# Optimization experiments

Hardware: AMD Instinct MI355X
Metric: run time of the kernel (lower is better)

The kernel has to match this reference:

```python
import jax, jax.numpy as jnp
import numpy as np

N = 100000   # total nodes in batched graph
E = 400000   # directed edges
F0 = 64      # Drug_Features
B = 512      # number of graphs
FINAL = 128  # Final_dim


def setup_inputs() -> dict:
    key = jax.random.key(0)
    ks = jax.random.split(key, 24)
    def w(k, shape, fan_in):
        return jax.random.normal(k, shape, dtype=jnp.float32) / np.sqrt(fan_in)
    inp = {
        "x": jax.random.normal(ks[0], (N, F0), dtype=jnp.float32),
        "edge_index": jax.random.randint(ks[1], (2, E), 0, N, dtype=jnp.int32),
        "batch": jnp.sort(jax.random.randint(ks[2], (N,), 0, B, dtype=jnp.int32)),
        "eps": jax.random.normal(ks[3], (N, 4 * F0), dtype=jnp.float32),
        # GCNConv weights: lin (in,out) no bias, separate bias added post-aggregation
        "W1": w(ks[4], (F0, 2 * F0), F0), "b1": jnp.zeros((2 * F0,), jnp.float32),
        "W2": w(ks[5], (2 * F0, 3 * F0), 2 * F0), "b2": jnp.zeros((3 * F0,), jnp.float32),
        "W3": w(ks[6], (3 * F0, 4 * F0), 3 * F0), "b3": jnp.zeros((4 * F0,), jnp.float32),
        "Wmu": w(ks[7], (4 * F0, 4 * F0), 4 * F0), "bmu": jnp.zeros((4 * F0,), jnp.float32),
        "Wlv": w(ks[8], (4 * F0, 4 * F0), 4 * F0), "blv": jnp.zeros((4 * F0,), jnp.float32),
        "fc1_w": w(ks[9], (4 * F0, 1024), 4 * F0), "fc1_b": jnp.zeros((1024,), jnp.float32),
        "fc2_w": w(ks[10], (1024, FINAL), 1024), "fc2_b": jnp.zeros((FINAL,), jnp.float32),
    }
    return inp


def reference(x, edge_index, batch, eps, W1, b1, W2, b2, W3, b3, Wmu, bmu, Wlv, blv,
              fc1_w, fc1_b, fc2_w, fc2_b):
    n = x.shape[0]
    row, col = edge_index[0], edge_index[1]
    loop = jnp.arange(n, dtype=row.dtype)
    row_f = jnp.concatenate([row, loop])  # with self-loops (PyG GCNConv default)
    col_f = jnp.concatenate([col, loop])
    deg = jax.ops.segment_sum(jnp.ones_like(col_f, dtype=x.dtype), col_f, num_segments=n)
    dinv = jnp.where(deg > 0, deg ** -0.5, 0.0)
    norm = (dinv[row_f] * dinv[col_f])[:, None]  # [E+N, 1]

    def gcn(h, W, b):
        m = h @ W                                   # transform first (out <= in here ok)
        agg = jax.ops.segment_sum(norm * m[row_f], col_f, num_segments=n)
        return agg + b

    h = jax.nn.relu(gcn(x, W1, b1))
    h = jax.nn.relu(gcn(h, W2, b2))
    h = jax.nn.relu(gcn(h, W3, b3))   # PMVO pre-pool features [N, 4F]
    mu = gcn(h, Wmu, bmu)
    logvar = gcn(h, Wlv, blv)
    std = jnp.exp(0.5 * logvar)
    amvo = mu + eps * std             # reparameterize
    x2 = jax.ops.segment_max(h, batch, num_segments=B)   # global max pool per graph
    pmvo = jax.nn.relu(x2 @ fc1_w + fc1_b) @ fc2_w + fc2_b  # dropout is identity (eval)
    return (amvo, mu, logvar, pmvo)
```

## Files before the change

kernel.cpp:

```cpp
#include <hip/hip_runtime.h>
#include <hip/hip_bf16.h>
#include <math.h>


#define THREADS 256

typedef short s8v __attribute__((ext_vector_type(8)));
typedef float f4v __attribute__((ext_vector_type(4)));

__device__ inline float bf_lo(unsigned int u) {
    union { unsigned int i; float f; } c; c.i = u << 16; return c.f;
}
__device__ inline float bf_hi(unsigned int u) {
    union { unsigned int i; float f; } c; c.i = u & 0xffff0000u; return c.f;
}
__device__ inline unsigned short f2bf(float f) {
    __hip_bfloat16 h = __float2bfloat16(f);
    return *reinterpret_cast<unsigned short*>(&h);
}
__device__ inline float bf2f(unsigned short u) {
    union { unsigned int i; float f; } c; c.i = ((unsigned int)u) << 16; return c.f;
}


__global__ void k_count(const int* __restrict__ col, int* __restrict__ counts, int E) {
    int e = blockIdx.x * blockDim.x + threadIdx.x;
    if (e < E) atomicAdd(&counts[col[e]], 1);
}

__global__ void k_dinv(const int* __restrict__ counts, float* __restrict__ dinv, int N) {
    int i = blockIdx.x * blockDim.x + threadIdx.x;
    if (i < N) dinv[i] = rsqrtf((float)(counts[i] + 1));
}

__global__ __launch_bounds__(1024) void k_scan(const int* __restrict__ counts,
                                               int* __restrict__ offsets, int N) {
    __shared__ int ssum[1024];
    int tid = threadIdx.x;
    int chunk = (N + 1023) / 1024;
    int begin = tid * chunk;
    int end = begin + chunk; if (end > N) end = N;
    int s = 0;
    for (int i = begin; i < end; ++i) s += counts[i] + 1;
    ssum[tid] = s;
    __syncthreads();
    for (int off = 1; off < 1024; off <<= 1) {
        int v = 0;
        if (tid >= off) v = ssum[tid - off];
        __syncthreads();
        if (tid >= off) ssum[tid] += v;
        __syncthreads();
    }
    int prefix = (tid == 0) ? 0 : ssum[tid - 1];
    for (int i = begin; i < end; ++i) {
        offsets[i] = prefix;
        prefix += counts[i] + 1;
    }
    if (end == N && begin < N) offsets[N] = prefix;
}

__global__ void k_init_cursor(const int* __restrict__ offsets, int* __restrict__ cursor, int N) {
    int i = blockIdx.x * blockDim.x + threadIdx.x;
    if (i < N) cursor[i] = offsets[i];
}

__global__ void k_scatter(const int* __restrict__ row, const int* __restrict__ col,
                          const float* __restrict__ dinv, int* __restrict__ cursor,
                          int* __restrict__ csr_row, float* __restrict__ csr_norm,
                          int E, int N) {
    int e = blockIdx.x * blockDim.x + threadIdx.x;
    if (e < E) {
        int r = row[e], c = col[e];
        int slot = atomicAdd(&cursor[c], 1);
        csr_row[slot] = r;
        csr_norm[slot] = dinv[r] * dinv[c];
    } else if (e < E + N) {
        int i = e - E;
        int slot = atomicAdd(&cursor[i], 1);
        csr_row[slot] = i;
        float d = dinv[i];
        csr_norm[slot] = d * d;
    }
}


__global__ void k_cast_bf16(const float* __restrict__ src, unsigned short* __restrict__ dst, int n) {
    int i = blockIdx.x * blockDim.x + threadIdx.x;
    if (i < n) dst[i] = f2bf(src[i]);
}

__global__ void k_prep_w(const float* __restrict__ W, unsigned short* __restrict__ WT,
                         int K, int Nc) {
    int id = blockIdx.x * blockDim.x + threadIdx.x;
    if (id < K * Nc) {
        int k = id / Nc, n = id % Nc;
        WT[(size_t)n * K + k] = f2bf(W[id]);
    }
}

__global__ void k_agg(const unsigned short* __restrict__ h,
                      const int* __restrict__ offsets,
                      const int* __restrict__ csr_row,
                      const float* __restrict__ csr_nrm,
                      unsigned short* __restrict__ g, int N, int F) {
    int node = blockIdx.x * blockDim.y + threadIdx.y;
    if (node >= N) return;
    int c8 = threadIdx.x * 8;
    int off0 = offsets[node], off1 = offsets[node + 1];
    float a0=0.f,a1=0.f,a2=0.f,a3=0.f,a4=0.f,a5=0.f,a6=0.f,a7=0.f;
    for (int sl = off0; sl < off1; ++sl) {
        int r = csr_row[sl];
        float w = csr_nrm[sl];
        uint4 v = *(const uint4*)(h + (size_t)r * F + c8);
        a0 += w * bf_lo(v.x); a1 += w * bf_hi(v.x);
        a2 += w * bf_lo(v.y); a3 += w * bf_hi(v.y);
        a4 += w * bf_lo(v.z); a5 += w * bf_hi(v.z);
        a6 += w * bf_lo(v.w); a7 += w * bf_hi(v.w);
    }
    uint4 o;
    o.x = (unsigned)f2bf(a0) | ((unsigned)f2bf(a1) << 16);
    o.y = (unsigned)f2bf(a2) | ((unsigned)f2bf(a3) << 16);
    o.z = (unsigned)f2bf(a4) | ((unsigned)f2bf(a5) << 16);
    o.w = (unsigned)f2bf(a6) | ((unsigned)f2bf(a7) << 16);
    *(uint4*)(g + (size_t)node * F + c8) = o;
}

#define GBM 128
#define GBN 64
#define GBK 64
#define LDP 72

__global__ __launch_bounds__(256) void k_gemm_mfma(
    const unsigned short* __restrict__ A,
    const unsigned short* __restrict__ WT,
    const float* __restrict__ bias,
    void* __restrict__ Cout, int M, int K, int Nc,
    int dorelu, int out_bf16) {
    __shared__ unsigned short sA[GBM * LDP];
    __shared__ unsigned short sB[GBN * LDP];
    const int tid = threadIdx.x;
    const int wave = tid >> 6;
    const int lane = tid & 63;
    const int bm = blockIdx.x * GBM;
    const int bn = blockIdx.y * GBN;

    f4v acc[2][4];
    #pragma unroll
    for (int i = 0; i < 2; ++i)
        #pragma unroll
        for (int j = 0; j < 4; ++j) acc[i][j] = (f4v){0.f, 0.f, 0.f, 0.f};

    const int lrow = tid >> 3;
    const int lk = (tid & 7) * 8;
    const int fr = lane & 15;
    const int fk = (lane >> 4) * 8;

    for (int k0 = 0; k0 < K; k0 += GBK) {
        #pragma unroll
        for (int p = 0; p < 4; ++p) {
            int r = lrow + p * 32;
            int gm = bm + r;
            uint4 v = make_uint4(0u, 0u, 0u, 0u);
            if (gm < M) v = *(const uint4*)(A + (size_t)gm * K + k0 + lk);
            *(uint4*)(&sA[r * LDP + lk]) = v;
        }
        #pragma unroll
        for (int p = 0; p < 2; ++p) {
            int n = lrow + p * 32;
            uint4 v = *(const uint4*)(WT + (size_t)(bn + n) * K + k0 + lk);
            *(uint4*)(&sB[n * LDP + lk]) = v;
        }
        __syncthreads();
        #pragma unroll
        for (int ks = 0; ks < 2; ++ks) {
            s8v a0 = *(const s8v*)(&sA[(wave * 32 + fr) * LDP + ks * 32 + fk]);
            s8v a1 = *(const s8v*)(&sA[(wave * 32 + 16 + fr) * LDP + ks * 32 + fk]);
            #pragma unroll
            for (int nt = 0; nt < 4; ++nt) {
                s8v b = *(const s8v*)(&sB[(nt * 16 + fr) * LDP + ks * 32 + fk]);
                acc[0][nt] = __builtin_amdgcn_mfma_f32_16x16x32_bf16(a0, b, acc[0][nt], 0, 0, 0);
                acc[1][nt] = __builtin_amdgcn_mfma_f32_16x16x32_bf16(a1, b, acc[1][nt], 0, 0, 0);
            }
        }
        __syncthreads();
    }

    const int col_l = lane & 15;
    const int row_q = (lane >> 4) * 4;
    #pragma unroll
    for (int mt = 0; mt < 2; ++mt) {
        #pragma unroll
        for (int nt = 0; nt < 4; ++nt) {
            #pragma unroll
            for (int i = 0; i < 4; ++i) {
                int row = bm + wave * 32 + mt * 16 + row_q + i;
                int col = bn + nt * 16 + col_l;
                if (row < M) {
                    float v = acc[mt][nt][i] + bias[col];
                    if (dorelu) v = fmaxf(v, 0.f);
                    if (out_bf16)
                        ((unsigned short*)Cout)[(size_t)row * Nc + col] = f2bf(v);
                    else
                        ((float*)Cout)[(size_t)row * Nc + col] = v;
                }
            }
        }
    }
}

__global__ __launch_bounds__(256) void k_fc1(const float* __restrict__ x2,
                                             const float* __restrict__ W,
                                             const float* __restrict__ bias,
                                             float* __restrict__ hid,
                                             int K, int Nc) {
    const int m = blockIdx.x;
    const int t = threadIdx.x;
    __shared__ float sx[256];
    for (int k = t; k < K; k += 256) sx[k] = x2[(size_t)m * K + k];
    __syncthreads();
    const int nc4 = Nc >> 2;
    const float4* Wv = (const float4*)W;
    float4 acc = make_float4(0.f, 0.f, 0.f, 0.f);
    #pragma unroll 4
    for (int k = 0; k < K; ++k) {
        float a = sx[k];
        float4 w = Wv[(size_t)k * nc4 + t];
        acc.x += a * w.x; acc.y += a * w.y;
        acc.z += a * w.z; acc.w += a * w.w;
    }
    float4 b = ((const float4*)bias)[t];
    float4 r;
    r.x = fmaxf(acc.x + b.x, 0.f);
    r.y = fmaxf(acc.y + b.y, 0.f);
    r.z = fmaxf(acc.z + b.z, 0.f);
    r.w = fmaxf(acc.w + b.w, 0.f);
    ((float4*)hid)[(size_t)m * nc4 + t] = r;
}

__global__ __launch_bounds__(128) void k_fc2(const float* __restrict__ hid,
                                             const float* __restrict__ W,
                                             const float* __restrict__ bias,
                                             float* __restrict__ out,
                                             int K, int Nc) {
    const int m = blockIdx.x;
    const int c = threadIdx.x;
    __shared__ float sh[1024];
    for (int k = c; k < K; k += 128) sh[k] = hid[(size_t)m * K + k];
    __syncthreads();
    float a0 = 0.f, a1 = 0.f, a2 = 0.f, a3 = 0.f;
    for (int k = 0; k < K; k += 4) {
        a0 += sh[k    ] * W[(size_t)(k    ) * Nc + c];
        a1 += sh[k + 1] * W[(size_t)(k + 1) * Nc + c];
        a2 += sh[k + 2] * W[(size_t)(k + 2) * Nc + c];
        a3 += sh[k + 3] * W[(size_t)(k + 3) * Nc + c];
    }
    out[(size_t)m * Nc + c] = (a0 + a1) + (a2 + a3) + bias[c];
}


__global__ void k_amvo(const float* __restrict__ mu, const float* __restrict__ lv,
                       const float* __restrict__ eps, float* __restrict__ out, size_t n) {
    size_t i = (size_t)blockIdx.x * blockDim.x + threadIdx.x;
    if (i < n) out[i] = mu[i] + eps[i] * expf(0.5f * lv[i]);
}

__global__ void k_gstart(const int* __restrict__ batch, int* __restrict__ gstart, int Nn, int B) {
    int b = blockIdx.x * blockDim.x + threadIdx.x;
    if (b > B) return;
    int lo = 0, hi = Nn;
    while (lo < hi) {
        int mid = (lo + hi) >> 1;
        if (batch[mid] < b) lo = mid + 1; else hi = mid;
    }
    gstart[b] = lo;
}

__global__ void k_pool_max(const unsigned short* __restrict__ h, const int* __restrict__ gstart,
                           float* __restrict__ x2, int F) {
    int b = blockIdx.x;
    int s = gstart[b], e = gstart[b + 1];
    for (int c = threadIdx.x; c < F; c += blockDim.x) {
        float mv = -INFINITY;
        for (int i = s; i < e; ++i) mv = fmaxf(mv, bf2f(h[(size_t)i * F + c]));
        x2[(size_t)b * F + c] = mv;
    }
}

static inline int ceil_div(int a, int b) { return (a + b - 1) / b; }

extern "C" void kernel_launch(void* const* d_in, const int* in_sizes, int n_in,
                              void* d_out, int out_size, void* d_ws, size_t ws_size,
                              hipStream_t stream) {
    const int F0 = 64;
    const int N = in_sizes[0] / F0;
    const int E = in_sizes[1] / 2;
    const int F4 = 4 * F0;
    const int B = (out_size - 3 * N * F4) / 128;
    const int M = E + N;

    const float* x     = (const float*)d_in[0];
    const int*   ei    = (const int*)d_in[1];
    const int*   batch = (const int*)d_in[2];
    const float* eps   = (const float*)d_in[3];
    const float* W1  = (const float*)d_in[4];  const float* b1  = (const float*)d_in[5];
    const float* W2  = (const float*)d_in[6];  const float* b2  = (const float*)d_in[7];
    const float* W3  = (const float*)d_in[8];  const float* b3  = (const float*)d_in[9];
    const float* Wmu = (const float*)d_in[10]; const float* bmu = (const float*)d_in[11];
    const float* Wlv = (const float*)d_in[12]; const float* blv = (const float*)d_in[13];
    const float* fc1w = (const float*)d_in[14]; const float* fc1b = (const float*)d_in[15];
    const float* fc2w = (const float*)d_in[16]; const float* fc2b = (const float*)d_in[17];

    const int* e_row = ei;
    const int* e_col = ei + E;

    float* out  = (float*)d_out;
    float* amvo = out;
    float* mu   = out + (size_t)N * F4;
    float* lv   = out + 2 * (size_t)N * F4;
    float* pmvo = out + 3 * (size_t)N * F4;

    char* w = (char*)d_ws;
    auto alloc = [&](size_t bytes) -> void* {
        void* p = (void*)w;
        w += (bytes + 255) & ~(size_t)255;
        return p;
    };
    float* dinv    = (float*)alloc((size_t)N * 4);
    int*   counts  = (int*)alloc((size_t)N * 4);
    int*   offsets = (int*)alloc((size_t)(N + 1) * 4);
    int*   csr_row = (int*)alloc((size_t)M * 4);
    float* csr_nrm = (float*)alloc((size_t)M * 4);
    int*   gstart  = (int*)alloc((size_t)(B + 1) * 4);
    unsigned short* xb  = (unsigned short*)alloc((size_t)N * F0 * 2);
    unsigned short* h1  = (unsigned short*)alloc((size_t)N * 128 * 2);
    unsigned short* h2  = (unsigned short*)alloc((size_t)N * 192 * 2);
    unsigned short* h3  = (unsigned short*)alloc((size_t)N * 256 * 2);
    unsigned short* g   = (unsigned short*)alloc((size_t)N * 256 * 2);
    unsigned short* wt1 = (unsigned short*)alloc((size_t)64 * 128 * 2);
    unsigned short* wt2 = (unsigned short*)alloc((size_t)128 * 192 * 2);
    unsigned short* wt3 = (unsigned short*)alloc((size_t)192 * 256 * 2);
    unsigned short* wtm = (unsigned short*)alloc((size_t)256 * 256 * 2);
    unsigned short* wtl = (unsigned short*)alloc((size_t)256 * 256 * 2);
    float* x2  = (float*)alloc((size_t)B * F4 * 4);
    float* hid = (float*)alloc((size_t)B * 1024 * 4);
    (void)ws_size; (void)n_in;

    hipMemsetAsync(counts, 0, (size_t)N * 4, stream);
    k_count<<<ceil_div(E, THREADS), THREADS, 0, stream>>>(e_col, counts, E);
    k_dinv<<<ceil_div(N, THREADS), THREADS, 0, stream>>>(counts, dinv, N);
    k_scan<<<1, 1024, 0, stream>>>(counts, offsets, N);
    k_init_cursor<<<ceil_div(N, THREADS), THREADS, 0, stream>>>(offsets, counts, N);
    k_scatter<<<ceil_div(E + N, THREADS), THREADS, 0, stream>>>(
        e_row, e_col, dinv, counts, csr_row, csr_nrm, E, N);

    k_cast_bf16<<<ceil_div(N * F0, THREADS), THREADS, 0, stream>>>(x, xb, N * F0);
    k_prep_w<<<ceil_div(64 * 128, THREADS), THREADS, 0, stream>>>(W1, wt1, 64, 128);
    k_prep_w<<<ceil_div(128 * 192, THREADS), THREADS, 0, stream>>>(W2, wt2, 128, 192);
    k_prep_w<<<ceil_div(192 * 256, THREADS), THREADS, 0, stream>>>(W3, wt3, 192, 256);
    k_prep_w<<<ceil_div(256 * 256, THREADS), THREADS, 0, stream>>>(Wmu, wtm, 256, 256);
    k_prep_w<<<ceil_div(256 * 256, THREADS), THREADS, 0, stream>>>(Wlv, wtl, 256, 256);

    {
        dim3 blk(8, 32);
        k_agg<<<ceil_div(N, 32), blk, 0, stream>>>(xb, offsets, csr_row, csr_nrm, g, N, 64);
        dim3 gg(ceil_div(N, GBM), 128 / GBN);
        k_gemm_mfma<<<gg, 256, 0, stream>>>(g, wt1, b1, h1, N, 64, 128, 1, 1);
    }
    {
        dim3 blk(16, 16);
        k_agg<<<ceil_div(N, 16), blk, 0, stream>>>(h1, offsets, csr_row, csr_nrm, g, N, 128);
        dim3 gg(ceil_div(N, GBM), 192 / GBN);
        k_gemm_mfma<<<gg, 256, 0, stream>>>(g, wt2, b2, h2, N, 128, 192, 1, 1);
    }
    {
        dim3 blk(24, 8);
        k_agg<<<ceil_div(N, 8), blk, 0, stream>>>(h2, offsets, csr_row, csr_nrm, g, N, 192);
        dim3 gg(ceil_div(N, GBM), 256 / GBN);
        k_gemm_mfma<<<gg, 256, 0, stream>>>(g, wt3, b3, h3, N, 192, 256, 1, 1);
    }
    {
        dim3 blk(32, 8);
        k_agg<<<ceil_div(N, 8), blk, 0, stream>>>(h3, offsets, csr_row, csr_nrm, g, N, 256);
        dim3 gg(ceil_div(N, GBM), 256 / GBN);
        k_gemm_mfma<<<gg, 256, 0, stream>>>(g, wtm, bmu, mu, N, 256, 256, 0, 0);
        k_gemm_mfma<<<gg, 256, 0, stream>>>(g, wtl, blv, lv, N, 256, 256, 0, 0);
    }

    {
        size_t n = (size_t)N * F4;
        k_amvo<<<(int)((n + THREADS - 1) / THREADS), THREADS, 0, stream>>>(mu, lv, eps, amvo, n);
    }

    k_gstart<<<ceil_div(B + 1, THREADS), THREADS, 0, stream>>>(batch, gstart, N, B);
    k_pool_max<<<B, 256, 0, stream>>>(h3, gstart, x2, F4);
    k_fc1<<<B, 256, 0, stream>>>(x2, fc1w, fc1b, hid, F4, 1024);
    k_fc2<<<B, 128, 0, stream>>>(hid, fc2w, fc2b, pmvo, 1024, 128);
}
```

Before: 1.198 ms.

## Fuse mu/logvar GEMMs with reparameterization and parallelize max pooling

```diff
diff --git a/kernel.cpp b/kernel.cpp
--- a/kernel.cpp
+++ b/kernel.cpp
@@ -202,6 +202,100 @@
                         ((unsigned short*)Cout)[(size_t)row * Nc + col] = f2bf(v);
                     else
                         ((float*)Cout)[(size_t)row * Nc + col] = v;
+                }
+            }
+        }
+    }
+}
+
+__global__ __launch_bounds__(256) void k_gemm_mfma_dual(
+    const unsigned short* __restrict__ A,
+    const unsigned short* __restrict__ WTm,
+    const unsigned short* __restrict__ WTl,
+    const float* __restrict__ bmu,
+    const float* __restrict__ blv,
+    const float* __restrict__ eps,
+    float* __restrict__ mu,
+    float* __restrict__ lv,
+    float* __restrict__ amvo,
+    int M, int K, int Nc) {
+    __shared__ unsigned short sA[GBM * LDP];
+    __shared__ unsigned short sBm[GBN * LDP];
+    __shared__ unsigned short sBl[GBN * LDP];
+    const int tid = threadIdx.x;
+    const int wave = tid >> 6;
+    const int lane = tid & 63;
+    const int bm = blockIdx.x * GBM;
+    const int bn = blockIdx.y * GBN;
+
+    f4v accM[2][4], accL[2][4];
+    #pragma unroll
+    for (int i = 0; i < 2; ++i)
+        #pragma unroll
+        for (int j = 0; j < 4; ++j) {
+            accM[i][j] = (f4v){0.f, 0.f, 0.f, 0.f};
+            accL[i][j] = (f4v){0.f, 0.f, 0.f, 0.f};
+        }
+
+    const int lrow = tid >> 3;
+    const int lk = (tid & 7) * 8;
+    const int fr = lane & 15;
+    const int fk = (lane >> 4) * 8;
+
+    for (int k0 = 0; k0 < K; k0 += GBK) {
+        #pragma unroll
+        for (int p = 0; p < 4; ++p) {
+            int r = lrow + p * 32;
+            int gm = bm + r;
+            uint4 v = make_uint4(0u, 0u, 0u, 0u);
+            if (gm < M) v = *(const uint4*)(A + (size_t)gm * K + k0 + lk);
+            *(uint4*)(&sA[r * LDP + lk]) = v;
+        }
+        #pragma unroll
+        for (int p = 0; p < 2; ++p) {
+            int n = lrow + p * 32;
+            uint4 vm = *(const uint4*)(WTm + (size_t)(bn + n) * K + k0 + lk);
+            uint4 vl = *(const uint4*)(WTl + (size_t)(bn + n) * K + k0 + lk);
+            *(uint4*)(&sBm[n * LDP + lk]) = vm;
+            *(uint4*)(&sBl[n * LDP + lk]) = vl;
+        }
+        __syncthreads();
+        #pragma unroll
+        for (int ks = 0; ks < 2; ++ks) {
+            s8v a0 = *(const s8v*)(&sA[(wave * 32 + fr) * LDP + ks * 32 + fk]);
+            s8v a1 = *(const s8v*)(&sA[(wave * 32 + 16 + fr) * LDP + ks * 32 + fk]);
+            #pragma unroll
+            for (int nt = 0; nt < 4; ++nt) {
+                s8v bm_ = *(const s8v*)(&sBm[(nt * 16 + fr) * LDP + ks * 32 + fk]);
+                s8v bl_ = *(const s8v*)(&sBl[(nt * 16 + fr) * LDP + ks * 32 + fk]);
+                accM[0][nt] = __builtin_amdgcn_mfma_f32_16x16x32_bf16(a0, bm_, accM[0][nt], 0, 0, 0);
+                accM[1][nt] = __builtin_amdgcn_mfma_f32_16x16x32_bf16(a1, bm_, accM[1][nt], 0, 0, 0);
+                accL[0][nt] = __builtin_amdgcn_mfma_f32_16x16x32_bf16(a0, bl_, accL[0][nt], 0, 0, 0);
+                accL[1][nt] = __builtin_amdgcn_mfma_f32_16x16x32_bf16(a1, bl_, accL[1][nt], 0, 0, 0);
+            }
+        }
+        __syncthreads();
+    }
+
+    const int col_l = lane & 15;
+    const int row_q = (lane >> 4) * 4;
+    #pragma unroll
+    for (int mt = 0; mt < 2; ++mt) {
+        #pragma unroll
+        for (int nt = 0; nt < 4; ++nt) {
+            int col = bn + nt * 16 + col_l;
+            float bM = bmu[col];
+            float bL = blv[col];
+            #pragma unroll
+            for (int i = 0; i < 4; ++i) {
+                int row = bm + wave * 32 + mt * 16 + row_q + i;
+                if (row < M) {
+                    size_t idx = (size_t)row * Nc + col;
+                    float vm = accM[mt][nt][i] + bM;
+                    float vl = accL[mt][nt][i] + bL;
+                    mu[idx] = vm;
+                    lv[idx] = vl;
+                    amvo[idx] = vm + eps[idx] * expf(0.5f * vl);
                 }
             }
         }
@@ -258,12 +352,6 @@
 }
 
 
-__global__ void k_amvo(const float* __restrict__ mu, const float* __restrict__ lv,
-                       const float* __restrict__ eps, float* __restrict__ out, size_t n) {
-    size_t i = (size_t)blockIdx.x * blockDim.x + threadIdx.x;
-    if (i < n) out[i] = mu[i] + eps[i] * expf(0.5f * lv[i]);
-}
-
 __global__ void k_gstart(const int* __restrict__ batch, int* __restrict__ gstart, int Nn, int B) {
     int b = blockIdx.x * blockDim.x + threadIdx.x;
     if (b > B) return;
@@ -278,10 +366,17 @@
 __global__ void k_pool_max(const unsigned short* __restrict__ h, const int* __restrict__ gstart,
                            float* __restrict__ x2, int F) {
     int b = blockIdx.x;
+    int c = blockIdx.y * 64 + threadIdx.x;
     int s = gstart[b], e = gstart[b + 1];
-    for (int c = threadIdx.x; c < F; c += blockDim.x) {
-        float mv = -INFINITY;
-        for (int i = s; i < e; ++i) mv = fmaxf(mv, bf2f(h[(size_t)i * F + c]));
+    float mv = -INFINITY;
+    for (int i = s + threadIdx.y; i < e; i += 4)
+        mv = fmaxf(mv, bf2f(h[(size_t)i * F + c]));
+    __shared__ float red[4][64];
+    red[threadIdx.y][threadIdx.x] = mv;
+    __syncthreads();
+    if (threadIdx.y == 0) {
+        mv = fmaxf(fmaxf(red[0][threadIdx.x], red[1][threadIdx.x]),
+                   fmaxf(red[2][threadIdx.x], red[3][threadIdx.x]));
         x2[(size_t)b * F + c] = mv;
     }
 }
@@ -382,17 +477,16 @@
         dim3 blk(32, 8);
         k_agg<<<ceil_div(N, 8), blk, 0, stream>>>(h3, offsets, csr_row, csr_nrm, g, N, 256);
         dim3 gg(ceil_div(N, GBM), 256 / GBN);
-        k_gemm_mfma<<<gg, 256, 0, stream>>>(g, wtm, bmu, mu, N, 256, 256, 0, 0);
-        k_gemm_mfma<<<gg, 256, 0, stream>>>(g, wtl, blv, lv, N, 256, 256, 0, 0);
-    }
-
+        k_gemm_mfma_dual<<<gg, 256, 0, stream>>>(g, wtm, wtl, bmu, blv, eps,
+                                                 mu, lv, amvo, N, 256, 256);
+    }
+
+    k_gstart<<<ceil_div(B + 1, THREADS), THREADS, 0, stream>>>(batch, gstart, N, B);
     {
-        size_t n = (size_t)N * F4;
-        k_amvo<<<(int)((n + THREADS - 1) / THREADS), THREADS, 0, stream>>>(mu, lv, eps, amvo, n);
-    }
-
-    k_gstart<<<ceil_div(B + 1, THREADS), THREADS, 0, stream>>>(batch, gstart, N, B);
-    k_pool_max<<<B, 256, 0, stream>>>(h3, gstart, x2, F4);
+        dim3 gg(B, F4 / 64);
+        dim3 blk(64, 4);
+        k_pool_max<<<gg, blk, 0, stream>>>(h3, gstart, x2, F4);
+    }
     k_fc1<<<B, 256, 0, stream>>>(x2, fc1w, fc1b, hid, F4, 1024);
     k_fc2<<<B, 128, 0, stream>>>(hid, fc2w, fc2b, pmvo, 1024, 128);
 }
```

Result: faster. 1.153 ms (-3.7%).
